# Kernel tuning notes

Hardware: AMD Instinct MI355X
Metric: run time of the kernel (lower is better)

## Reference

```python
import jax, jax.numpy as jnp
import numpy as np

B = 128        # batch (images/texts)
N = 2048       # other texts per image
F_IMG = 1024   # raw image feature dim (abstracted encoder input)
F_TXT = 512    # raw text feature dim
D = 512        # embedding dim (num_features=512 in BasicNet)
TOPK = B - 1   # default topK = batch - 1


def setup_inputs() -> dict:
    key = jax.random.key(0)
    ks = jax.random.split(key, 6)
    return {
        "input_images": jax.random.normal(ks[0], (B, F_IMG), jnp.float32),
        "input_texts": jax.random.normal(ks[1], (B, F_TXT), jnp.float32),
        "other_texts": jax.random.normal(ks[2], (B, N, F_TXT), jnp.float32),
        "W_img": jax.random.normal(ks[3], (F_IMG, D), jnp.float32) / np.float32(np.sqrt(F_IMG)),
        "W_txt": jax.random.normal(ks[4], (F_TXT, D), jnp.float32) / np.float32(np.sqrt(F_TXT)),
        "logit_scale": jnp.asarray(np.log(1.0 / 0.07), jnp.float32),
    }


def reference(input_images, input_texts, other_texts, W_img, W_txt, logit_scale):
    K = TOPK
    # encoders abstracted as linear projections to D=512
    img = input_images @ W_img                                   # [B, D]
    img = img / jnp.linalg.norm(img, axis=1, keepdims=True)      # L2-normalize images
    txt = input_texts @ W_txt                                    # [B, D]
    txt = txt / jnp.linalg.norm(txt, axis=1, keepdims=True)      # row-wise norm == norm after concat
    oth = jnp.einsum('bnf,fd->bnd', other_texts, W_txt)          # [B, N, D]
    oth = oth / jnp.linalg.norm(oth, axis=2, keepdims=True)

    scale = jnp.exp(logit_scale)
    logit_in = scale * jnp.sum(img * txt, axis=1)                # [B] image_i . text_i
    logit_oth = scale * jnp.einsum('bd,bnd->bn', img, oth)       # [B, N]

    # descending sort + take top-K (lax.top_k returns sorted descending)
    topk_vals, _ = jax.lax.top_k(logit_oth, K)                   # [B, K]

    # indices = sorted(range(K) + [min(i, K-1)]): duplicate element p=min(i,K-1)
    rows = jnp.arange(B)
    cols = jnp.arange(K + 1)[None, :]                            # [1, K+1]
    p = jnp.minimum(rows, K - 1)[:, None]                        # [B, 1]
    gidx = jnp.where(cols <= p, cols, cols - 1)                  # [B, K+1]
    gathered = jnp.take_along_axis(topk_vals, gidx, axis=1)      # [B, K+1]

    # overwrite column i of row i with the positive (input text) logit
    out = jnp.where(cols == rows[:, None], logit_in[:, None], gathered)
    return out
```

## Files before the change

### kernel.cpp

```cpp
#include <hip/hip_runtime.h>
#include <math.h>

#define B_SZ 128
#define N_OTH 2048
#define F_IMG 1024
#define F_TXT 512
#define D_EMB 512

typedef __attribute__((ext_vector_type(8))) short short8;
typedef __attribute__((ext_vector_type(4))) float f32x4;

static __device__ __forceinline__ ushort f2bf(float f) {
    union { float f; unsigned u; } v; v.f = f;
    unsigned u = v.u;
    return (ushort)((u + 0x7fffu + ((u >> 16) & 1u)) >> 16);
}

__global__ __launch_bounds__(512) void k_img(const float* __restrict__ in_img,
                                             const float* __restrict__ W,
                                             float* __restrict__ img) {
    const int b = blockIdx.x;
    const int d = threadIdx.x;
    __shared__ float row[F_IMG];
    __shared__ float wsum[8];
    __shared__ float s_rn;
    for (int i = d; i < F_IMG; i += 512) row[i] = in_img[b * F_IMG + i];
    __syncthreads();
    float acc = 0.f;
#pragma unroll 8
    for (int f = 0; f < F_IMG; ++f) acc = fmaf(row[f], W[f * D_EMB + d], acc);
    float sq = acc * acc;
#pragma unroll
    for (int off = 32; off > 0; off >>= 1) sq += __shfl_down(sq, off);
    const int lane = d & 63, wv = d >> 6;
    if (lane == 0) wsum[wv] = sq;
    __syncthreads();
    if (d == 0) {
        float s = 0.f;
        for (int w = 0; w < 8; ++w) s += wsum[w];
        s_rn = 1.0f / sqrtf(s);
    }
    __syncthreads();
    img[b * D_EMB + d] = acc * s_rn;
}

__global__ __launch_bounds__(512) void k_txt(const float* __restrict__ in_txt,
                                             const float* __restrict__ W,
                                             const float* __restrict__ img,
                                             const float* __restrict__ p_ls,
                                             float* __restrict__ logit_in) {
    const int b = blockIdx.x;
    const int d = threadIdx.x;
    __shared__ float row[F_TXT];
    __shared__ float wsum[8];
    __shared__ float s_rn;
    row[d] = in_txt[b * F_TXT + d];
    __syncthreads();
    float acc = 0.f;
#pragma unroll 8
    for (int f = 0; f < F_TXT; ++f) acc = fmaf(row[f], W[f * D_EMB + d], acc);
    float sq = acc * acc;
#pragma unroll
    for (int off = 32; off > 0; off >>= 1) sq += __shfl_down(sq, off);
    const int lane = d & 63, wv = d >> 6;
    if (lane == 0) wsum[wv] = sq;
    __syncthreads();
    if (d == 0) {
        float s = 0.f;
        for (int w = 0; w < 8; ++w) s += wsum[w];
        s_rn = 1.0f / sqrtf(s);
    }
    __syncthreads();
    const float t = acc * s_rn;
    float pd = t * img[b * D_EMB + d];
#pragma unroll
    for (int off = 32; off > 0; off >>= 1) pd += __shfl_down(pd, off);
    __syncthreads();
    if (lane == 0) wsum[wv] = pd;
    __syncthreads();
    if (d == 0) {
        float s = 0.f;
        for (int w = 0; w < 8; ++w) s += wsum[w];
        logit_in[b] = expf(p_ls[0]) * s;
    }
}

__global__ __launch_bounds__(256) void k_wprep(const float* __restrict__ W,
                                               ushort* __restrict__ wf) {
    const int g = blockIdx.x * 256 + threadIdx.x;
    const int lane = g & 63;
    const int frag = g >> 6;
    const int kstep = frag >> 5;
    const int ct = frag & 31;
    const int d = ct * 16 + (lane & 15);
    const int kb = kstep * 32 + (lane >> 4) * 8;
    short8 o;
#pragma unroll
    for (int j = 0; j < 8; ++j) o[j] = (short)f2bf(W[(kb + j) * D_EMB + d]);
    *(short8*)(wf + (size_t)g * 8) = o;
}

__global__ __launch_bounds__(512) void k_gemm(const float* __restrict__ oth,
                                              const ushort* __restrict__ wf,
                                              const float* __restrict__ img,
                                              float* __restrict__ numA,
                                              float* __restrict__ denA) {
    __shared__ ushort sA[2][64 * 32];
    __shared__ float redN[8][64];
    __shared__ float redD[8][64];
    const int tid = threadIdx.x;
    const int l = tid & 63;
    const int wv = tid >> 6;
    const int b = blockIdx.x >> 5;
    const size_t row0 = (size_t)blockIdx.x * 64;

    const int srow = tid >> 3;
    const int sk4 = (tid & 7) * 4;
    const float* gsrc = oth + (row0 + srow) * F_TXT + sk4;
    const int swb = (srow * 64 + sk4 * 2) ^ ((srow & 7) << 4);

    f32x4 acc[4][4];
#pragma unroll
    for (int m = 0; m < 4; ++m)
#pragma unroll
        for (int n = 0; n < 4; ++n) acc[m][n] = (f32x4){0.f, 0.f, 0.f, 0.f};

    {
        float4 v = *(const float4*)gsrc;
        ushort4 p;
        p.x = f2bf(v.x); p.y = f2bf(v.y); p.z = f2bf(v.z); p.w = f2bf(v.w);
        *(ushort4*)((char*)sA[0] + swb) = p;
    }
    __syncthreads();

    int abase[4];
#pragma unroll
    for (int m = 0; m < 4; ++m)
        abase[m] = (((m * 16 + (l & 15)) * 64 + (l >> 4) * 16) ^ ((l & 7) << 4));

    float4 nv;
    for (int s = 0; s < 16; ++s) {
        const int cur = s & 1;
        if (s < 15) nv = *(const float4*)(gsrc + (s + 1) * 32);
        short8 bf[4];
#pragma unroll
        for (int n = 0; n < 4; ++n)
            bf[n] = *(const short8*)(wf + (((size_t)(s * 32 + wv * 4 + n)) * 64 + l) * 8);
        short8 af[4];
#pragma unroll
        for (int m = 0; m < 4; ++m)
            af[m] = *(const short8*)((const char*)sA[cur] + abase[m]);
#pragma unroll
        for (int m = 0; m < 4; ++m)
#pragma unroll
            for (int n = 0; n < 4; ++n)
                acc[m][n] = __builtin_amdgcn_mfma_f32_16x16x32_bf16(af[m], bf[n], acc[m][n], 0, 0, 0);
        __syncthreads();
        if (s < 15) {
            ushort4 p;
            p.x = f2bf(nv.x); p.y = f2bf(nv.y); p.z = f2bf(nv.z); p.w = f2bf(nv.w);
            *(ushort4*)((char*)sA[cur ^ 1] + swb) = p;
        }
        __syncthreads();
    }

    float icol[4];
#pragma unroll
    for (int n = 0; n < 4; ++n)
        icol[n] = img[b * D_EMB + wv * 64 + n * 16 + (l & 15)];
#pragma unroll
    for (int m = 0; m < 4; ++m) {
#pragma unroll
        for (int r = 0; r < 4; ++r) {
            float tn = 0.f, td = 0.f;
#pragma unroll
            for (int n = 0; n < 4; ++n) {
                float p = acc[m][n][r];
                tn = fmaf(p, icol[n], tn);
                td = fmaf(p, p, td);
            }
#pragma unroll
            for (int off = 1; off <= 8; off <<= 1) {
                tn += __shfl_xor(tn, off);
                td += __shfl_xor(td, off);
            }
            if ((l & 15) == 0) {
                const int row = m * 16 + (l >> 4) * 4 + r;
                redN[wv][row] = tn;
                redD[wv][row] = td;
            }
        }
    }
    __syncthreads();
    if (tid < 64) {
        float tn = 0.f, td = 0.f;
#pragma unroll
        for (int w = 0; w < 8; ++w) { tn += redN[w][tid]; td += redD[w][tid]; }
        numA[row0 + tid] = tn;
        denA[row0 + tid] = td;
    }
}

__global__ __launch_bounds__(256) void k_topk(const float* __restrict__ numA,
                                              const float* __restrict__ denA,
                                              const float* __restrict__ logit_in,
                                              const float* __restrict__ p_ls,
                                              float* __restrict__ out) {
    const int b = blockIdx.x;
    const int tid = threadIdx.x;
    const float scale = expf(p_ls[0]);
    __shared__ float a[N_OTH];
    for (int i = tid; i < N_OTH; i += 256) {
        const float nu = numA[(size_t)b * N_OTH + i];
        const float de = denA[(size_t)b * N_OTH + i];
        a[i] = scale * nu / sqrtf(de);
    }
    __syncthreads();
    for (unsigned k = 2; k <= N_OTH; k <<= 1) {
        for (unsigned j = k >> 1; j > 0; j >>= 1) {
            for (int s = 0; s < N_OTH / 256; ++s) {
                const unsigned i = tid + s * 256u;
                const unsigned ixj = i ^ j;
                if (ixj > i) {
                    const bool asc = ((i & k) == 0);
                    const float x = a[i], y = a[ixj];
                    if ((x > y) == asc) { a[i] = y; a[ixj] = x; }
                }
            }
            __syncthreads();
        }
    }
    if (tid < 128) {
        const int j = tid;
        float v;
        if (j == b) {
            v = logit_in[b];
        } else {
            const int m = j - (j > b ? 1 : 0);
            v = a[N_OTH - 1 - m];
        }
        out[b * 128 + j] = v;
    }
}

extern "C" void kernel_launch(void* const* d_in, const int* in_sizes, int n_in,
                              void* d_out, int out_size, void* d_ws, size_t ws_size,
                              hipStream_t stream) {
    const float* in_img = (const float*)d_in[0];
    const float* in_txt = (const float*)d_in[1];
    const float* oth    = (const float*)d_in[2];
    const float* W_img  = (const float*)d_in[3];
    const float* W_txt  = (const float*)d_in[4];
    const float* p_ls   = (const float*)d_in[5];
    float* out = (float*)d_out;

    float* ws = (float*)d_ws;
    float* img      = ws;
    float* logit_in = ws + 65536;
    float* numA     = ws + 65536 + 128;
    float* denA     = numA + 262144;
    ushort* wfrag   = (ushort*)(denA + 262144);

    k_wprep<<<128, 256, 0, stream>>>(W_txt, wfrag);
    k_img<<<B_SZ, 512, 0, stream>>>(in_img, W_img, img);
    k_txt<<<B_SZ, 512, 0, stream>>>(in_txt, W_txt, img, p_ls, logit_in);
    k_gemm<<<(B_SZ * N_OTH) / 64, 512, 0, stream>>>(oth, wfrag, img, numA, denA);
    k_topk<<<B_SZ, 256, 0, stream>>>(numA, denA, logit_in, p_ls, out);
}
```

Measured before the change: 376.1 us.

## Use 128-row tiles with 32x32x16 MFMA and a deeper K step in the GEMM

The projection GEMM over other_texts now uses 128-row blocks instead of 64, switches from 16x16x32 to 32x32x16 bf16 MFMA, and advances 64 K-columns per pipeline stage. The weight fragment prep is re-laid-out to match the new MFMA operand format. This halves the number of barriers per K and loads each weight fragment once per 128 rows instead of per 64. The cost is more LDS per block (32KB double buffer) and more accumulator registers, which can cut occupancy.

```diff
diff --git a/kernel.cpp b/kernel.cpp
--- a/kernel.cpp
+++ b/kernel.cpp
@@ -8,7 +8,7 @@
 #define D_EMB 512
 
 typedef __attribute__((ext_vector_type(8))) short short8;
-typedef __attribute__((ext_vector_type(4))) float f32x4;
+typedef __attribute__((ext_vector_type(16))) float f32x16;
 
 static __device__ __forceinline__ ushort f2bf(float f) {
     union { float f; unsigned u; } v; v.f = f;
@@ -88,111 +88,120 @@
 __global__ __launch_bounds__(256) void k_wprep(const float* __restrict__ W,
                                                ushort* __restrict__ wf) {
     const int g = blockIdx.x * 256 + threadIdx.x;
-    const int lane = g & 63;
+    const int l = g & 63;
     const int frag = g >> 6;
-    const int kstep = frag >> 5;
-    const int ct = frag & 31;
-    const int d = ct * 16 + (lane & 15);
-    const int kb = kstep * 32 + (lane >> 4) * 8;
+    const int kstep = frag >> 4;
+    const int ct = frag & 15;
+    const int col = ct * 32 + (l & 31);
+    const int kb = kstep * 16 + (l >> 5) * 8;
     short8 o;
 #pragma unroll
-    for (int j = 0; j < 8; ++j) o[j] = (short)f2bf(W[(kb + j) * D_EMB + d]);
+    for (int j = 0; j < 8; ++j) o[j] = (short)f2bf(W[(kb + j) * D_EMB + col]);
     *(short8*)(wf + (size_t)g * 8) = o;
 }
 
-__global__ __launch_bounds__(512) void k_gemm(const float* __restrict__ oth,
-                                              const ushort* __restrict__ wf,
-                                              const float* __restrict__ img,
-                                              float* __restrict__ numA,
-                                              float* __restrict__ denA) {
-    __shared__ ushort sA[2][64 * 32];
-    __shared__ float redN[8][64];
-    __shared__ float redD[8][64];
+__global__ __launch_bounds__(512, 2) void k_gemm(const float* __restrict__ oth,
+                                                 const ushort* __restrict__ wf,
+                                                 const float* __restrict__ img,
+                                                 float* __restrict__ numA,
+                                                 float* __restrict__ denA) {
+    __shared__ ushort sA[2][128 * 64];
+    __shared__ float redN[8][128];
+    __shared__ float redD[8][128];
     const int tid = threadIdx.x;
     const int l = tid & 63;
     const int wv = tid >> 6;
-    const int b = blockIdx.x >> 5;
-    const size_t row0 = (size_t)blockIdx.x * 64;
-
-    const int srow = tid >> 3;
-    const int sk4 = (tid & 7) * 4;
-    const float* gsrc = oth + (row0 + srow) * F_TXT + sk4;
-    const int swb = (srow * 64 + sk4 * 2) ^ ((srow & 7) << 4);
-
-    f32x4 acc[4][4];
+    const int b = blockIdx.x >> 4;
+    const size_t row0 = (size_t)blockIdx.x * 128;
+
+    const int srow = tid >> 4;
+    const int sc = tid & 15;
+    const float* gbase = oth + row0 * F_TXT;
+
+    f32x16 acc[4][2];
 #pragma unroll
     for (int m = 0; m < 4; ++m)
 #pragma unroll
-        for (int n = 0; n < 4; ++n) acc[m][n] = (f32x4){0.f, 0.f, 0.f, 0.f};
-
-    {
-        float4 v = *(const float4*)gsrc;
+        for (int n = 0; n < 2; ++n)
+#pragma unroll
+            for (int r = 0; r < 16; ++r) acc[m][n][r] = 0.f;
+
+    float4 nv[4];
+#pragma unroll
+    for (int i = 0; i < 4; ++i)
+        nv[i] = *(const float4*)(gbase + (size_t)(srow + i * 32) * F_TXT + sc * 4);
+#pragma unroll
+    for (int i = 0; i < 4; ++i) {
+        const int r = srow + i * 32;
         ushort4 p;
-        p.x = f2bf(v.x); p.y = f2bf(v.y); p.z = f2bf(v.z); p.w = f2bf(v.w);
-        *(ushort4*)((char*)sA[0] + swb) = p;
-    }
-    __syncthreads();
-
-    int abase[4];
-#pragma unroll
-    for (int m = 0; m < 4; ++m)
-        abase[m] = (((m * 16 + (l & 15)) * 64 + (l >> 4) * 16) ^ ((l & 7) << 4));
-
-    float4 nv;
-    for (int s = 0; s < 16; ++s) {
-        const int cur = s & 1;
-        if (s < 15) nv = *(const float4*)(gsrc + (s + 1) * 32);
-        short8 bf[4];
-#pragma unroll
-        for (int n = 0; n < 4; ++n)
-            bf[n] = *(const short8*)(wf + (((size_t)(s * 32 + wv * 4 + n)) * 64 + l) * 8);
-        short8 af[4];
-#pragma unroll
-        for (int m = 0; m < 4; ++m)
-            af[m] = *(const short8*)((const char*)sA[cur] + abase[m]);
-#pragma unroll
-        for (int m = 0; m < 4; ++m)
-#pragma unroll
-            for (int n = 0; n < 4; ++n)
-                acc[m][n] = __builtin_amdgcn_mfma_f32_16x16x32_bf16(af[m], bf[n], acc[m][n], 0, 0, 0);
+        p.x = f2bf(nv[i].x); p.y = f2bf(nv[i].y); p.z = f2bf(nv[i].z); p.w = f2bf(nv[i].w);
+        *(ushort4*)((char*)sA[0] + r * 128 + ((sc * 8) ^ ((r & 7) << 4))) = p;
+    }
+
+    for (int t = 0; t < 8; ++t) {
+        const int cur = t & 1;
         __syncthreads();
-        if (s < 15) {
-            ushort4 p;
-            p.x = f2bf(nv.x); p.y = f2bf(nv.y); p.z = f2bf(nv.z); p.w = f2bf(nv.w);
-            *(ushort4*)((char*)sA[cur ^ 1] + swb) = p;
-        }
-        __syncthreads();
-    }
-
-    float icol[4];
-#pragma unroll
-    for (int n = 0; n < 4; ++n)
-        icol[n] = img[b * D_EMB + wv * 64 + n * 16 + (l & 15)];
+        if (t < 7) {
+#pragma unroll
+            for (int i = 0; i < 4; ++i)
+                nv[i] = *(const float4*)(gbase + (size_t)(srow + i * 32) * F_TXT + (t + 1) * 64 + sc * 4);
+        }
+        short8 bfr[4][2];
+#pragma unroll
+        for (int ks = 0; ks < 4; ++ks)
+#pragma unroll
+            for (int n = 0; n < 2; ++n)
+                bfr[ks][n] = *(const short8*)(wf + (((size_t)((t * 4 + ks) * 16 + wv * 2 + n)) * 64 + l) * 8);
+#pragma unroll
+        for (int ks = 0; ks < 4; ++ks) {
+            short8 af[4];
+#pragma unroll
+            for (int m = 0; m < 4; ++m) {
+                const int r = m * 32 + (l & 31);
+                af[m] = *(const short8*)((const char*)sA[cur] + r * 128 +
+                                         ((ks * 32 + (l >> 5) * 16) ^ ((r & 7) << 4)));
+            }
+#pragma unroll
+            for (int m = 0; m < 4; ++m)
+#pragma unroll
+                for (int n = 0; n < 2; ++n)
+                    acc[m][n] = __builtin_amdgcn_mfma_f32_32x32x16_bf16(af[m], bfr[ks][n], acc[m][n], 0, 0, 0);
+        }
+        if (t < 7) {
+#pragma unroll
+            for (int i = 0; i < 4; ++i) {
+                const int r = srow + i * 32;
+                ushort4 p;
+                p.x = f2bf(nv[i].x); p.y = f2bf(nv[i].y); p.z = f2bf(nv[i].z); p.w = f2bf(nv[i].w);
+                *(ushort4*)((char*)sA[cur ^ 1] + r * 128 + ((sc * 8) ^ ((r & 7) << 4))) = p;
+            }
+        }
+    }
+
+    const float ic0 = img[b * D_EMB + wv * 64 + (l & 31)];
+    const float ic1 = img[b * D_EMB + wv * 64 + 32 + (l & 31)];
 #pragma unroll
     for (int m = 0; m < 4; ++m) {
 #pragma unroll
-        for (int r = 0; r < 4; ++r) {
-            float tn = 0.f, td = 0.f;
-#pragma unroll
-            for (int n = 0; n < 4; ++n) {
-                float p = acc[m][n][r];
-                tn = fmaf(p, icol[n], tn);
-                td = fmaf(p, p, td);
-            }
-#pragma unroll
-            for (int off = 1; off <= 8; off <<= 1) {
+        for (int rg = 0; rg < 16; ++rg) {
+            const float p = acc[m][0][rg];
+            const float q = acc[m][1][rg];
+            float tn = p * ic0 + q * ic1;
+            float td = p * p + q * q;
+#pragma unroll
+            for (int off = 1; off <= 16; off <<= 1) {
                 tn += __shfl_xor(tn, off);
                 td += __shfl_xor(td, off);
             }
-            if ((l & 15) == 0) {
-                const int row = m * 16 + (l >> 4) * 4 + r;
-                redN[wv][row] = tn;
-                redD[wv][row] = td;
-            }
-        }
-    }
-    __syncthreads();
-    if (tid < 64) {
+            if ((l & 31) == 0) {
+                const int r = m * 32 + (rg & 3) + 8 * (rg >> 2) + 4 * (l >> 5);
+                redN[wv][r] = tn;
+                redD[wv][r] = td;
+            }
+        }
+    }
+    __syncthreads();
+    if (tid < 128) {
         float tn = 0.f, td = 0.f;
 #pragma unroll
         for (int w = 0; w < 8; ++w) { tn += redN[w][tid]; td += redD[w][tid]; }
@@ -264,6 +273,6 @@
     k_wprep<<<128, 256, 0, stream>>>(W_txt, wfrag);
     k_img<<<B_SZ, 512, 0, stream>>>(in_img, W_img, img);
     k_txt<<<B_SZ, 512, 0, stream>>>(in_txt, W_txt, img, p_ls, logit_in);
-    k_gemm<<<(B_SZ * N_OTH) / 64, 512, 0, stream>>>(oth, wfrag, img, numA, denA);
+    k_gemm<<<(B_SZ * N_OTH) / 128, 512, 0, stream>>>(oth, wfrag, img, numA, denA);
     k_topk<<<B_SZ, 256, 0, stream>>>(numA, denA, logit_in, p_ls, out);
 }
```

Result: slower. 474.4 us (+26.1%).
